# Performance work log

Measured on AMD Instinct MI355X. Metric: run time of the kernel, lower is better.

The kernel has to match this reference:

```python
import jax, jax.numpy as jnp
import numpy as np

N, E, HD, ED = 8000, 40000, 64, 16


def setup_inputs() -> dict:
    key = jax.random.key(0)
    ks = jax.random.split(key, 10)
    def nrm(k, shp, s):
        return jax.random.normal(k, shp, dtype=jnp.float32) * s
    return {
        "x": jax.random.normal(ks[0], (N, HD), dtype=jnp.float32),
        "edge_attr": jax.random.uniform(ks[1], (E, ED), dtype=jnp.float32),
        "W1": nrm(ks[2], (ED, HD), 0.2),
        "b1": jnp.zeros((HD,), jnp.float32),
        "W2": nrm(ks[3], (HD, HD * HD), 0.05),
        "b2": jnp.zeros((HD * HD,), jnp.float32),
        "W_root": nrm(ks[4], (HD, HD), 0.1),
        "b_conv": jnp.zeros((HD,), jnp.float32),
        "w_ih": nrm(ks[5], (3 * HD, HD), 0.1),
        "w_hh": nrm(ks[6], (3 * HD, HD), 0.1),
        "b_ih": jnp.zeros((3 * HD,), jnp.float32),
        "b_hh": jnp.zeros((3 * HD,), jnp.float32),
        "edge_index": jax.random.randint(ks[7], (2, E), 0, N),
    }


def reference(x, edge_attr, W1, b1, W2, b2, W_root, b_conv, w_ih, w_hh, b_ih, b_hh, edge_index):
    src, dst = edge_index[0], edge_index[1]
    n_nodes, hd = x.shape
    n_edges = edge_attr.shape[0]
    # in-degree counts for scatter-mean (guard against isolated nodes)
    counts = jnp.maximum(
        jax.ops.segment_sum(jnp.ones((n_edges,), x.dtype), dst, num_segments=n_nodes), 1.0
    )
    # edge MLP -> per-edge [hd, hd] weight; edge_attr is loop-invariant so compute once
    Wedge = (jax.nn.relu(edge_attr @ W1 + b1) @ W2 + b2).reshape(n_edges, hd, hd)

    def gru_cell(m, h):
        gi = m @ w_ih.T + b_ih  # [N, 3h], gate order r,z,n (torch layout)
        gh = h @ w_hh.T + b_hh
        i_r, i_z, i_n = jnp.split(gi, 3, axis=-1)
        h_r, h_z, h_n = jnp.split(gh, 3, axis=-1)
        r = jax.nn.sigmoid(i_r + h_r)
        z = jax.nn.sigmoid(i_z + h_z)
        n = jnp.tanh(i_n + r * h_n)
        return (1.0 - z) * n + z * h

    out = x
    hidden = x  # h = out.unsqueeze(0)
    for _ in range(3):
        # NNConv: gather source feats, per-edge matmul, scatter-mean to target
        msg = jnp.einsum('ei,eio->eo', out[src], Wedge)  # [E, hd]
        agg = jax.ops.segment_sum(msg, dst, num_segments=n_nodes) / counts[:, None]
        m = jax.nn.relu(agg + out @ W_root.T + b_conv)
        hidden = gru_cell(m, hidden)
        out = hidden  # GRU output == new hidden for seq_len 1
    return out
```

## Files before the change

kernel.cpp:

```cpp
#include <hip/hip_runtime.h>

#define HD 64
#define ED 16
#define NB 16
#define OSTR 144
#define NSTR 9232
#define LDSB (NB*NSTR)
#define GSTR 201

typedef __bf16 bf16x8 __attribute__((ext_vector_type(8)));
typedef float  f32x4  __attribute__((ext_vector_type(4)));
typedef unsigned int u32;
typedef unsigned long long u64;
typedef unsigned short u16;

static inline __device__ float bf2f(u16 u){
    union { u32 i; float f; } v; v.i = ((u32)u) << 16; return v.f;
}
static inline __device__ u16 f2bf(float f){
    union { u32 i; float f; } v; v.f = f;
    u32 r = v.i + 0x7FFF + ((v.i >> 16) & 1);
    return (u16)(r >> 16);
}
static inline __device__ u32 pk2(float a, float b){
    return (u32)f2bf(a) | ((u32)f2bf(b) << 16);
}

__global__ void k_zero2(int* a, int* b, int n){
    int i = blockIdx.x*blockDim.x + threadIdx.x;
    if(i < n){ a[i] = 0; b[i] = 0; }
}
__global__ void k_zerof(float* a, int n){
    int i = blockIdx.x*blockDim.x + threadIdx.x;
    if(i < n) a[i] = 0.f;
}
__global__ void k_deg(const int* __restrict__ src, const int* __restrict__ dst, int E,
                      int* __restrict__ degs, int* __restrict__ degd){
    int e = blockIdx.x*blockDim.x + threadIdx.x;
    if(e < E){ atomicAdd(&degs[src[e]], 1); atomicAdd(&degd[dst[e]], 1); }
}

__global__ void k_scan(const int* __restrict__ degs, const int* __restrict__ degd, int N,
                       int* __restrict__ rowptr, int* __restrict__ cursor, float* __restrict__ countsf){
    __shared__ int part[1024];
    int tid = threadIdx.x;
    int PER = (N + 1023) >> 10;
    int base = tid * PER;
    int local[16];
    int s = 0;
    for(int j = 0; j < PER; j++){
        int idx = base + j;
        int v = (idx < N) ? degs[idx] : 0;
        local[j] = s; s += v;
    }
    part[tid] = s;
    __syncthreads();
    for(int off = 1; off < 1024; off <<= 1){
        int v = (tid >= off) ? part[tid - off] : 0;
        __syncthreads();
        part[tid] += v;
        __syncthreads();
    }
    int prev = (tid == 0) ? 0 : part[tid - 1];
    for(int j = 0; j < PER; j++){
        int idx = base + j;
        if(idx < N){
            int r = prev + local[j];
            rowptr[idx] = r; cursor[idx] = r;
            int dd = degd[idx];
            countsf[idx] = (dd > 0) ? (float)dd : 1.0f;
        }
    }
    if(tid == 1023) rowptr[N] = prev + s;
}

__global__ void k_fill(const int* __restrict__ src, int E, int* __restrict__ cursor, int* __restrict__ elist){
    int e = blockIdx.x*blockDim.x + threadIdx.x;
    if(e < E){ int p = atomicAdd(&cursor[src[e]], 1); elist[p] = e; }
}

__global__ void k_h1E(const float* __restrict__ ea, const float* __restrict__ W1,
                      const float* __restrict__ b1, const int* __restrict__ elist,
                      const int* __restrict__ dstarr, int E,
                      u16* __restrict__ h1E, int* __restrict__ dstE){
    __shared__ float s_ea[4][ED];
    __shared__ int s_e[4];
    int t = threadIdx.x;
    int o = t & 63, el = t >> 6;
    int p = blockIdx.x*4 + el;
    if(t < 4){
        int pp = blockIdx.x*4 + t;
        s_e[t] = (pp < E) ? elist[pp] : 0;
    }
    __syncthreads();
    if(t < 4*ED){
        int pe = t/ED;
        s_ea[pe][t%ED] = ea[(size_t)s_e[pe]*ED + t%ED];
    }
    __syncthreads();
    if(p < E){
        float acc = b1[o];
        #pragma unroll
        for(int k = 0; k < ED; k++) acc += s_ea[el][k] * W1[k*HD + o];
        h1E[(size_t)p*HD + o] = f2bf(acc > 0.f ? acc : 0.f);
        if(o == 0) dstE[p] = dstarr[s_e[el]];
    }
}

__global__ void k_permT(const float* __restrict__ W2, const float* __restrict__ b2,
                        u16* __restrict__ PT){
    int idx = blockIdx.x*blockDim.x + threadIdx.x;
    if(idx >= 65*HD*HD) return;
    int c = idx / HD, i = idx % HD;
    int kc = c >> 6, o = c & 63;
    float v = (kc < HD) ? W2[(size_t)kc*(HD*HD) + i*HD + o] : b2[i*HD + o];
    PT[idx] = f2bf(v);
}

__global__ void k_cvtA(const float* __restrict__ s, u16* __restrict__ a, int n){
    int i = (blockIdx.x*blockDim.x + threadIdx.x) * 4;
    if(i < n){
        float4 v = *(const float4*)&s[i];
        ushort4 o;
        o.x = f2bf(v.x); o.y = f2bf(v.y); o.z = f2bf(v.z); o.w = f2bf(v.w);
        *(ushort4*)&a[i] = o;
    }
}

__global__ __launch_bounds__(1024) void k_fused(
        const u16* __restrict__ Abf, const u16* __restrict__ PT,
        const u16* __restrict__ h1E, const int* __restrict__ rowptr,
        const int* __restrict__ dstE, int E, float* __restrict__ agg){
    extern __shared__ char smem[];
    int t = threadIdx.x;
    int w = t >> 6;
    int lane = t & 63;
    int r = lane & 15, g = lane >> 4;
    int nb0 = blockIdx.x * NB;

    bf16x8 afr0 = *(const bf16x8*)&Abf[(size_t)(nb0 + r)*HD + g*8];
    bf16x8 afr1 = *(const bf16x8*)&Abf[(size_t)(nb0 + r)*HD + 32 + g*8];
    {
        f32x4 acc[4][4];
        #pragma unroll
        for(int j = 0; j < 4; j++)
            #pragma unroll
            for(int cb = 0; cb < 4; cb++) acc[j][cb] = (f32x4){0.f,0.f,0.f,0.f};
        #pragma unroll
        for(int j = 0; j < 4; j++){
            int kc = 4*w + j;
            const u16* Pb = PT + (size_t)kc*HD*HD;
            #pragma unroll
            for(int cb = 0; cb < 4; cb++){
                bf16x8 b0 = *(const bf16x8*)&Pb[(size_t)(cb*16 + r)*HD + g*8];
                bf16x8 b1 = *(const bf16x8*)&Pb[(size_t)(cb*16 + r)*HD + 32 + g*8];
                acc[j][cb] = __builtin_amdgcn_mfma_f32_16x16x32_bf16(afr0, b0, acc[j][cb], 0,0,0);
                acc[j][cb] = __builtin_amdgcn_mfma_f32_16x16x32_bf16(afr1, b1, acc[j][cb], 0,0,0);
            }
        }
        #pragma unroll
        for(int cb = 0; cb < 4; cb++){
            int o = cb*16 + r;
            int slotp = ((w>>1) + 2*o + (o>>3)) & 7;
            #pragma unroll
            for(int reg = 0; reg < 4; reg++){
                int node = 4*g + reg;
                u32 lo = pk2(acc[0][cb][reg], acc[1][cb][reg]);
                u32 hi = pk2(acc[2][cb][reg], acc[3][cb][reg]);
                *(u64*)(smem + node*NSTR + o*OSTR + slotp*16 + 8*(w&1)) =
                    (u64)lo | ((u64)hi << 32);
            }
        }
        if(w == 0){
            f32x4 accB[4];
            #pragma unroll
            for(int cb = 0; cb < 4; cb++) accB[cb] = (f32x4){0.f,0.f,0.f,0.f};
            const u16* Pb = PT + (size_t)64*HD*HD;
            #pragma unroll
            for(int cb = 0; cb < 4; cb++){
                bf16x8 b0 = *(const bf16x8*)&Pb[(size_t)(cb*16 + r)*HD + g*8];
                bf16x8 b1 = *(const bf16x8*)&Pb[(size_t)(cb*16 + r)*HD + 32 + g*8];
                accB[cb] = __builtin_amdgcn_mfma_f32_16x16x32_bf16(afr0, b0, accB[cb], 0,0,0);
                accB[cb] = __builtin_amdgcn_mfma_f32_16x16x32_bf16(afr1, b1, accB[cb], 0,0,0);
            }
            #pragma unroll
            for(int cb = 0; cb < 4; cb++)
                #pragma unroll
                for(int reg = 0; reg < 4; reg++)
                    *(u16*)(smem + (4*g+reg)*NSTR + (cb*16+r)*OSTR + 128) =
                        f2bf(accB[cb][reg]);
        }
    }
    __syncthreads();

    int s = nb0 + w;
    int beg = rowptr[s], end = rowptr[s+1];
    if(beg == end) return;
    const char* nodebase = smem + w*NSTR;
    bf16x8 sB[4][2];
    float bval[4];
    #pragma unroll
    for(int cb = 0; cb < 4; cb++){
        int o = cb*16 + r;
        #pragma unroll
        for(int ks = 0; ks < 2; ks++){
            int slotp = ((ks*4 + g) + 2*o + (o>>3)) & 7;
            sB[cb][ks] = *(const bf16x8*)(nodebase + o*OSTR + slotp*16);
        }
        bval[cb] = bf2f(*(const u16*)(nodebase + o*OSTR + 128));
    }
    for(int p0 = beg; p0 < end; p0 += 16){
        int p = p0 + r;
        int pc = p < E ? p : E-1;
        bf16x8 a0 = *(const bf16x8*)&h1E[(size_t)pc*HD + g*8];
        bf16x8 a1 = *(const bf16x8*)&h1E[(size_t)pc*HD + 32 + g*8];
        f32x4 acc2[4];
        #pragma unroll
        for(int cb = 0; cb < 4; cb++){
            acc2[cb] = (f32x4){0.f,0.f,0.f,0.f};
            acc2[cb] = __builtin_amdgcn_mfma_f32_16x16x32_bf16(a0, sB[cb][0], acc2[cb], 0,0,0);
            acc2[cb] = __builtin_amdgcn_mfma_f32_16x16x32_bf16(a1, sB[cb][1], acc2[cb], 0,0,0);
        }
        int dq[4];
        #pragma unroll
        for(int reg = 0; reg < 4; reg++){
            int q = p0 + 4*g + reg;
            dq[reg] = (q < end) ? dstE[q] : -1;
        }
        #pragma unroll
        for(int cb = 0; cb < 4; cb++)
            #pragma unroll
            for(int reg = 0; reg < 4; reg++)
                if(dq[reg] >= 0)
                    atomicAdd(&agg[(size_t)dq[reg]*HD + cb*16 + r],
                              acc2[cb][reg] + bval[cb]);
    }
}

__global__ __launch_bounds__(256) void k_mgru2(
        const float* __restrict__ agg, const float* __restrict__ countsf,
        const float* __restrict__ state, const u16* __restrict__ Abf,
        const u16* __restrict__ WrB,  const u16* __restrict__ WihB,
        const u16* __restrict__ WhhB, const float* __restrict__ bconv,
        const float* __restrict__ b_ih, const float* __restrict__ b_hh,
        float* __restrict__ hnew, u16* __restrict__ AbfN){
    __shared__ u16   s_mbf[16*72];
    __shared__ float s_gi[16*GSTR];
    __shared__ float s_gh[16*GSTR];
    int t = threadIdx.x;
    int w = t >> 6, lane = t & 63;
    int r = lane & 15, g = lane >> 4;
    int n0 = blockIdx.x * 16;

    bf16x8 afr0 = *(const bf16x8*)&Abf[(size_t)(n0 + r)*HD + g*8];
    bf16x8 afr1 = *(const bf16x8*)&Abf[(size_t)(n0 + r)*HD + 32 + g*8];

    {
        float bc = bconv[w*16 + r];
        f32x4 accR = (f32x4){bc, bc, bc, bc};
        bf16x8 b0 = *(const bf16x8*)&WrB[(size_t)(w*16 + r)*HD + g*8];
        bf16x8 b1 = *(const bf16x8*)&WrB[(size_t)(w*16 + r)*HD + 32 + g*8];
        accR = __builtin_amdgcn_mfma_f32_16x16x32_bf16(afr0, b0, accR, 0,0,0);
        accR = __builtin_amdgcn_mfma_f32_16x16x32_bf16(afr1, b1, accR, 0,0,0);
        #pragma unroll
        for(int reg = 0; reg < 4; reg++){
            int row = 4*g + reg;
            float cnt = countsf[n0 + row];
            float m = agg[(size_t)(n0 + row)*HD + w*16 + r] / cnt + accR[reg];
            s_mbf[row*72 + w*16 + r] = f2bf(m > 0.f ? m : 0.f);
        }
    }
    __syncthreads();

    bf16x8 am0 = *(const bf16x8*)&s_mbf[r*72 + g*8];
    bf16x8 am1 = *(const bf16x8*)&s_mbf[r*72 + 32 + g*8];

    #pragma unroll
    for(int j = 0; j < 3; j++){
        int cb = w + 4*j;
        int col = cb*16 + r;
        float bi = b_ih[col];
        f32x4 acc = (f32x4){bi, bi, bi, bi};
        bf16x8 b0 = *(const bf16x8*)&WihB[(size_t)col*HD + g*8];
        bf16x8 b1 = *(const bf16x8*)&WihB[(size_t)col*HD + 32 + g*8];
        acc = __builtin_amdgcn_mfma_f32_16x16x32_bf16(am0, b0, acc, 0,0,0);
        acc = __builtin_amdgcn_mfma_f32_16x16x32_bf16(am1, b1, acc, 0,0,0);
        #pragma unroll
        for(int reg = 0; reg < 4; reg++)
            s_gi[(4*g + reg)*GSTR + col] = acc[reg];
    }
    #pragma unroll
    for(int j = 0; j < 3; j++){
        int cb = w + 4*j;
        int col = cb*16 + r;
        float bh = b_hh[col];
        f32x4 acc = (f32x4){bh, bh, bh, bh};
        bf16x8 b0 = *(const bf16x8*)&WhhB[(size_t)col*HD + g*8];
        bf16x8 b1 = *(const bf16x8*)&WhhB[(size_t)col*HD + 32 + g*8];
        acc = __builtin_amdgcn_mfma_f32_16x16x32_bf16(afr0, b0, acc, 0,0,0);
        acc = __builtin_amdgcn_mfma_f32_16x16x32_bf16(afr1, b1, acc, 0,0,0);
        #pragma unroll
        for(int reg = 0; reg < 4; reg++)
            s_gh[(4*g + reg)*GSTR + col] = acc[reg];
    }
    __syncthreads();

    #pragma unroll
    for(int q = 0; q < 4; q++){
        int idx = t + q*256;
        int nl = idx >> 6, o = idx & 63;
        const float* gi = s_gi + nl*GSTR;
        const float* gh = s_gh + nl*GSTR;
        float rr  = 1.f/(1.f + __expf(-(gi[o]      + gh[o])));
        float zz  = 1.f/(1.f + __expf(-(gi[64+o]   + gh[64+o])));
        float nnv = tanhf(gi[128+o] + rr*gh[128+o]);
        float xo = state[(size_t)(n0+nl)*HD + o];
        float h = (1.f - zz)*nnv + zz*xo;
        hnew[(size_t)(n0+nl)*HD + o] = h;
        AbfN[(size_t)(n0+nl)*HD + o] = f2bf(h);
    }
}

extern "C" void kernel_launch(void* const* d_in, const int* in_sizes, int n_in,
                              void* d_out, int out_size, void* d_ws, size_t ws_size,
                              hipStream_t stream){
    const float* x     = (const float*)d_in[0];
    const float* ea    = (const float*)d_in[1];
    const float* W1    = (const float*)d_in[2];
    const float* b1    = (const float*)d_in[3];
    const float* W2    = (const float*)d_in[4];
    const float* b2    = (const float*)d_in[5];
    const float* Wroot = (const float*)d_in[6];
    const float* bconv = (const float*)d_in[7];
    const float* w_ih  = (const float*)d_in[8];
    const float* w_hh  = (const float*)d_in[9];
    const float* b_ih  = (const float*)d_in[10];
    const float* b_hh  = (const float*)d_in[11];
    const int*   eidx  = (const int*)d_in[12];
    int N = in_sizes[0] / HD;
    int E = in_sizes[1] / ED;
    const int* srcarr = eidx;
    const int* dstarr = eidx + E;

    char* w = (char*)d_ws;
    size_t off = 0;
    auto alloc = [&](size_t bytes)->char*{
        char* p = w + off; off = (off + bytes + 255) & ~(size_t)255; return p;
    };
    int*   deg_src = (int*)alloc((size_t)N*4);
    int*   deg_dst = (int*)alloc((size_t)N*4);
    int*   rowptr  = (int*)alloc((size_t)(N+1)*4);
    int*   cursor  = (int*)alloc((size_t)N*4);
    int*   elist   = (int*)alloc((size_t)E*4);
    int*   dstE    = (int*)alloc((size_t)E*4);
    float* countsf = (float*)alloc((size_t)N*4);
    u16*   h1E     = (u16*)alloc((size_t)E*HD*2);
    u16*   PT      = (u16*)alloc((size_t)65*HD*HD*2);
    u16*   Abf     = (u16*)alloc((size_t)N*HD*2);
    u16*   WihB    = (u16*)alloc((size_t)3*HD*HD*2);
    u16*   WhhB    = (u16*)alloc((size_t)3*HD*HD*2);
    u16*   WrB     = (u16*)alloc((size_t)HD*HD*2);
    float* agg     = (float*)alloc((size_t)N*HD*4);
    float* stA     = (float*)alloc((size_t)N*HD*4);
    float* stB     = (float*)alloc((size_t)N*HD*4);

    hipFuncSetAttribute((const void*)k_fused,
                        hipFuncAttributeMaxDynamicSharedMemorySize, LDSB);

    hipLaunchKernelGGL(k_zero2, dim3((N+255)/256), dim3(256), 0, stream, deg_src, deg_dst, N);
    hipLaunchKernelGGL(k_deg,   dim3((E+255)/256), dim3(256), 0, stream, srcarr, dstarr, E, deg_src, deg_dst);
    hipLaunchKernelGGL(k_scan,  dim3(1), dim3(1024), 0, stream, deg_src, deg_dst, N, rowptr, cursor, countsf);
    hipLaunchKernelGGL(k_fill,  dim3((E+255)/256), dim3(256), 0, stream, srcarr, E, cursor, elist);
    hipLaunchKernelGGL(k_h1E,   dim3((E+3)/4), dim3(256), 0, stream, ea, W1, b1, elist, dstarr, E, h1E, dstE);
    hipLaunchKernelGGL(k_permT, dim3((65*HD*HD+255)/256), dim3(256), 0, stream, W2, b2, PT);
    hipLaunchKernelGGL(k_cvtA,  dim3((3*HD*HD/4+255)/256), dim3(256), 0, stream, w_ih, WihB, 3*HD*HD);
    hipLaunchKernelGGL(k_cvtA,  dim3((3*HD*HD/4+255)/256), dim3(256), 0, stream, w_hh, WhhB, 3*HD*HD);
    hipLaunchKernelGGL(k_cvtA,  dim3((HD*HD/4+255)/256), dim3(256), 0, stream, Wroot, WrB, HD*HD);
    hipLaunchKernelGGL(k_cvtA,  dim3((N*HD/4+255)/256), dim3(256), 0, stream, x, Abf, N*HD);

    const float* state = x;
    for(int it = 0; it < 3; ++it){
        hipLaunchKernelGGL(k_zerof, dim3((N*HD+255)/256), dim3(256), 0, stream, agg, N*HD);
        hipLaunchKernelGGL(k_fused, dim3(N/NB), dim3(1024), LDSB, stream,
                           Abf, PT, h1E, rowptr, dstE, E, agg);
        float* outp = (it == 2) ? (float*)d_out : ((it == 0) ? stA : stB);
        hipLaunchKernelGGL(k_mgru2, dim3(N/16), dim3(256), 0, stream,
                           agg, countsf, state, Abf, WrB, WihB, WhhB,
                           bconv, b_ih, b_hh, outp, Abf);
        state = outp;
    }
}
```

Measured before the change: 222.1 us.

## Split fused NNConv kernel across two K-halves with 512-thread blocks

```diff
diff --git a/kernel.cpp b/kernel.cpp
--- a/kernel.cpp
+++ b/kernel.cpp
@@ -3,10 +3,9 @@
 #define HD 64
 #define ED 16
 #define NB 16
-#define OSTR 144
-#define NSTR 9232
-#define LDSB (NB*NSTR)
-#define GSTR 201
+#define OSTR2 72
+#define NSTR2 4616
+#define LDS2B (NB*NSTR2 + NB*HD*4)
 
 typedef __bf16 bf16x8 __attribute__((ext_vector_type(8)));
 typedef float  f32x4  __attribute__((ext_vector_type(4)));
@@ -127,16 +126,24 @@
     }
 }
 
-__global__ __launch_bounds__(1024) void k_fused(
+__global__ __launch_bounds__(512, 4) void k_fused2(
         const u16* __restrict__ Abf, const u16* __restrict__ PT,
         const u16* __restrict__ h1E, const int* __restrict__ rowptr,
         const int* __restrict__ dstE, int E, float* __restrict__ agg){
     extern __shared__ char smem[];
+    float* s_biasf = (float*)(smem + NB*NSTR2);
     int t = threadIdx.x;
     int w = t >> 6;
     int lane = t & 63;
     int r = lane & 15, g = lane >> 4;
-    int nb0 = blockIdx.x * NB;
+    int gb = blockIdx.x;
+    int grp = gb >> 1, h = gb & 1;
+    int nb0 = grp * NB;
+
+    int n0 = 2*w, n1 = 2*w + 1;
+    int beg0 = rowptr[nb0 + n0];
+    int beg1 = rowptr[nb0 + n1];
+    int end1 = rowptr[nb0 + n1 + 1];
 
     bf16x8 afr0 = *(const bf16x8*)&Abf[(size_t)(nb0 + r)*HD + g*8];
     bf16x8 afr1 = *(const bf16x8*)&Abf[(size_t)(nb0 + r)*HD + 32 + g*8];
@@ -148,7 +155,7 @@
             for(int cb = 0; cb < 4; cb++) acc[j][cb] = (f32x4){0.f,0.f,0.f,0.f};
         #pragma unroll
         for(int j = 0; j < 4; j++){
-            int kc = 4*w + j;
+            int kc = h*32 + 4*w + j;
             const u16* Pb = PT + (size_t)kc*HD*HD;
             #pragma unroll
             for(int cb = 0; cb < 4; cb++){
@@ -161,17 +168,16 @@
         #pragma unroll
         for(int cb = 0; cb < 4; cb++){
             int o = cb*16 + r;
-            int slotp = ((w>>1) + 2*o + (o>>3)) & 7;
             #pragma unroll
             for(int reg = 0; reg < 4; reg++){
                 int node = 4*g + reg;
                 u32 lo = pk2(acc[0][cb][reg], acc[1][cb][reg]);
                 u32 hi = pk2(acc[2][cb][reg], acc[3][cb][reg]);
-                *(u64*)(smem + node*NSTR + o*OSTR + slotp*16 + 8*(w&1)) =
+                *(u64*)(smem + node*NSTR2 + o*OSTR2 + w*8) =
                     (u64)lo | ((u64)hi << 32);
             }
         }
-        if(w == 0){
+        if(h == 1 && w == 0){
             f32x4 accB[4];
             #pragma unroll
             for(int cb = 0; cb < 4; cb++) accB[cb] = (f32x4){0.f,0.f,0.f,0.f};
@@ -187,56 +193,53 @@
             for(int cb = 0; cb < 4; cb++)
                 #pragma unroll
                 for(int reg = 0; reg < 4; reg++)
-                    *(u16*)(smem + (4*g+reg)*NSTR + (cb*16+r)*OSTR + 128) =
-                        f2bf(accB[cb][reg]);
-        }
-    }
-    __syncthreads();
-
-    int s = nb0 + w;
-    int beg = rowptr[s], end = rowptr[s+1];
-    if(beg == end) return;
-    const char* nodebase = smem + w*NSTR;
-    bf16x8 sB[4][2];
-    float bval[4];
+                    s_biasf[(4*g + reg)*HD + cb*16 + r] = accB[cb][reg];
+        }
+    }
+    __syncthreads();
+
     #pragma unroll
-    for(int cb = 0; cb < 4; cb++){
-        int o = cb*16 + r;
-        #pragma unroll
-        for(int ks = 0; ks < 2; ks++){
-            int slotp = ((ks*4 + g) + 2*o + (o>>3)) & 7;
-            sB[cb][ks] = *(const bf16x8*)(nodebase + o*OSTR + slotp*16);
-        }
-        bval[cb] = bf2f(*(const u16*)(nodebase + o*OSTR + 128));
-    }
-    for(int p0 = beg; p0 < end; p0 += 16){
-        int p = p0 + r;
-        int pc = p < E ? p : E-1;
-        bf16x8 a0 = *(const bf16x8*)&h1E[(size_t)pc*HD + g*8];
-        bf16x8 a1 = *(const bf16x8*)&h1E[(size_t)pc*HD + 32 + g*8];
-        f32x4 acc2[4];
+    for(int nn = 0; nn < 2; nn++){
+        int node = (nn == 0) ? n0 : n1;
+        int beg  = (nn == 0) ? beg0 : beg1;
+        int end  = (nn == 0) ? beg1 : end1;
+        if(beg == end) continue;
+        const char* nodebase = smem + node*NSTR2;
+        bf16x8 sB[4];
+        float bval[4];
         #pragma unroll
         for(int cb = 0; cb < 4; cb++){
-            acc2[cb] = (f32x4){0.f,0.f,0.f,0.f};
-            acc2[cb] = __builtin_amdgcn_mfma_f32_16x16x32_bf16(a0, sB[cb][0], acc2[cb], 0,0,0);
-            acc2[cb] = __builtin_amdgcn_mfma_f32_16x16x32_bf16(a1, sB[cb][1], acc2[cb], 0,0,0);
-        }
-        int dq[4];
-        #pragma unroll
-        for(int reg = 0; reg < 4; reg++){
-            int q = p0 + 4*g + reg;
-            dq[reg] = (q < end) ? dstE[q] : -1;
-        }
-        #pragma unroll
-        for(int cb = 0; cb < 4; cb++)
-            #pragma unroll
-            for(int reg = 0; reg < 4; reg++)
-                if(dq[reg] >= 0)
-                    atomicAdd(&agg[(size_t)dq[reg]*HD + cb*16 + r],
-                              acc2[cb][reg] + bval[cb]);
-    }
-}
-
+            sB[cb] = *(const bf16x8*)(nodebase + (cb*16 + r)*OSTR2 + g*16);
+            bval[cb] = (h == 1) ? s_biasf[node*HD + cb*16 + r] : 0.f;
+        }
+        for(int p0 = beg; p0 < end; p0 += 16){
+            int p = p0 + r;
+            int pc = p < E ? p : E-1;
+            bf16x8 a0 = *(const bf16x8*)&h1E[(size_t)pc*HD + h*32 + g*8];
+            f32x4 acc2[4];
+            #pragma unroll
+            for(int cb = 0; cb < 4; cb++){
+                acc2[cb] = (f32x4){0.f,0.f,0.f,0.f};
+                acc2[cb] = __builtin_amdgcn_mfma_f32_16x16x32_bf16(a0, sB[cb], acc2[cb], 0,0,0);
+            }
+            int dq[4];
+            #pragma unroll
+            for(int reg = 0; reg < 4; reg++){
+                int q = p0 + 4*g + reg;
+                dq[reg] = (q < end) ? dstE[q] : -1;
+            }
+            #pragma unroll
+            for(int cb = 0; cb < 4; cb++)
+                #pragma unroll
+                for(int reg = 0; reg < 4; reg++)
+                    if(dq[reg] >= 0)
+                        atomicAdd(&agg[(size_t)dq[reg]*HD + cb*16 + r],
+                                  acc2[cb][reg] + bval[cb]);
+        }
+    }
+}
+
+#define GSTR 201
 __global__ __launch_bounds__(256) void k_mgru2(
         const float* __restrict__ agg, const float* __restrict__ countsf,
         const float* __restrict__ state, const u16* __restrict__ Abf,
@@ -315,9 +318,9 @@
         float zz  = 1.f/(1.f + __expf(-(gi[64+o]   + gh[64+o])));
         float nnv = tanhf(gi[128+o] + rr*gh[128+o]);
         float xo = state[(size_t)(n0+nl)*HD + o];
-        float h = (1.f - zz)*nnv + zz*xo;
-        hnew[(size_t)(n0+nl)*HD + o] = h;
-        AbfN[(size_t)(n0+nl)*HD + o] = f2bf(h);
+        float hh = (1.f - zz)*nnv + zz*xo;
+        hnew[(size_t)(n0+nl)*HD + o] = hh;
+        AbfN[(size_t)(n0+nl)*HD + o] = f2bf(hh);
     }
 }
 
@@ -364,8 +367,8 @@
     float* stA     = (float*)alloc((size_t)N*HD*4);
     float* stB     = (float*)alloc((size_t)N*HD*4);
 
-    hipFuncSetAttribute((const void*)k_fused,
-                        hipFuncAttributeMaxDynamicSharedMemorySize, LDSB);
+    hipFuncSetAttribute((const void*)k_fused2,
+                        hipFuncAttributeMaxDynamicSharedMemorySize, LDS2B);
 
     hipLaunchKernelGGL(k_zero2, dim3((N+255)/256), dim3(256), 0, stream, deg_src, deg_dst, N);
     hipLaunchKernelGGL(k_deg,   dim3((E+255)/256), dim3(256), 0, stream, srcarr, dstarr, E, deg_src, deg_dst);
@@ -381,7 +384,7 @@
     const float* state = x;
     for(int it = 0; it < 3; ++it){
         hipLaunchKernelGGL(k_zerof, dim3((N*HD+255)/256), dim3(256), 0, stream, agg, N*HD);
-        hipLaunchKernelGGL(k_fused, dim3(N/NB), dim3(1024), LDSB, stream,
+        hipLaunchKernelGGL(k_fused2, dim3((N/NB)*2), dim3(512), LDS2B, stream,
                            Abf, PT, h1E, rowptr, dstE, E, agg);
         float* outp = (it == 2) ? (float*)d_out : ((it == 0) ? stA : stB);
         hipLaunchKernelGGL(k_mgru2, dim3(N/16), dim3(256), 0, stream,
```

Result: no change. 226.1 us (+1.8%).

## Split fused per-node GEMM and message kernel, staging node matrices in global memory

Applied to the files above, without the earlier changes.

```diff
diff --git a/kernel.cpp b/kernel.cpp
--- a/kernel.cpp
+++ b/kernel.cpp
@@ -2,11 +2,6 @@
 
 #define HD 64
 #define ED 16
-#define NB 16
-#define OSTR 144
-#define NSTR 9232
-#define LDSB (NB*NSTR)
-#define GSTR 201
 
 typedef __bf16 bf16x8 __attribute__((ext_vector_type(8)));
 typedef float  f32x4  __attribute__((ext_vector_type(4)));
@@ -127,87 +122,93 @@
     }
 }
 
-__global__ __launch_bounds__(1024) void k_fused(
+__global__ __launch_bounds__(256) void k_gemmA(
         const u16* __restrict__ Abf, const u16* __restrict__ PT,
+        u16* __restrict__ Mt){
+    int t = threadIdx.x;
+    int w = t >> 6, lane = t & 63;
+    int r = lane & 15, g = lane >> 4;
+    int kcq = blockIdx.x;
+    int n0 = (blockIdx.y * 4 + w) * 16;
+
+    bf16x8 a0 = *(const bf16x8*)&Abf[(size_t)(n0 + r)*HD + g*8];
+    bf16x8 a1 = *(const bf16x8*)&Abf[(size_t)(n0 + r)*HD + 32 + g*8];
+
+    f32x4 acc[8][4];
+    #pragma unroll
+    for(int j = 0; j < 8; j++)
+        #pragma unroll
+        for(int cb = 0; cb < 4; cb++) acc[j][cb] = (f32x4){0.f,0.f,0.f,0.f};
+
+    #pragma unroll
+    for(int j = 0; j < 8; j++){
+        const u16* Pb = PT + (size_t)(kcq*8 + j)*HD*HD;
+        #pragma unroll
+        for(int cb = 0; cb < 4; cb++){
+            bf16x8 b0 = *(const bf16x8*)&Pb[(cb*16 + r)*HD + g*8];
+            bf16x8 b1 = *(const bf16x8*)&Pb[(cb*16 + r)*HD + 32 + g*8];
+            acc[j][cb] = __builtin_amdgcn_mfma_f32_16x16x32_bf16(a0, b0, acc[j][cb], 0,0,0);
+            acc[j][cb] = __builtin_amdgcn_mfma_f32_16x16x32_bf16(a1, b1, acc[j][cb], 0,0,0);
+        }
+    }
+
+    #pragma unroll
+    for(int cb = 0; cb < 4; cb++)
+        #pragma unroll
+        for(int reg = 0; reg < 4; reg++){
+            int node = n0 + 4*g + reg;
+            uint4 val;
+            val.x = pk2(acc[0][cb][reg], acc[1][cb][reg]);
+            val.y = pk2(acc[2][cb][reg], acc[3][cb][reg]);
+            val.z = pk2(acc[4][cb][reg], acc[5][cb][reg]);
+            val.w = pk2(acc[6][cb][reg], acc[7][cb][reg]);
+            *(uint4*)&Mt[(size_t)node*4096 + (size_t)(kcq*64 + cb*16 + r)*8] = val;
+        }
+}
+
+__global__ __launch_bounds__(256) void k_biasA(
+        const u16* __restrict__ Abf, const u16* __restrict__ PT,
+        float* __restrict__ Mb){
+    int t = threadIdx.x;
+    int w = t >> 6, lane = t & 63;
+    int r = lane & 15, g = lane >> 4;
+    int n0 = (blockIdx.x * 4 + w) * 16;
+    bf16x8 a0 = *(const bf16x8*)&Abf[(size_t)(n0 + r)*HD + g*8];
+    bf16x8 a1 = *(const bf16x8*)&Abf[(size_t)(n0 + r)*HD + 32 + g*8];
+    const u16* Pb = PT + (size_t)64*HD*HD;
+    #pragma unroll
+    for(int cb = 0; cb < 4; cb++){
+        f32x4 acc = (f32x4){0.f,0.f,0.f,0.f};
+        bf16x8 b0 = *(const bf16x8*)&Pb[(cb*16 + r)*HD + g*8];
+        bf16x8 b1 = *(const bf16x8*)&Pb[(cb*16 + r)*HD + 32 + g*8];
+        acc = __builtin_amdgcn_mfma_f32_16x16x32_bf16(a0, b0, acc, 0,0,0);
+        acc = __builtin_amdgcn_mfma_f32_16x16x32_bf16(a1, b1, acc, 0,0,0);
+        #pragma unroll
+        for(int reg = 0; reg < 4; reg++)
+            Mb[(size_t)(n0 + 4*g + reg)*HD + cb*16 + r] = acc[reg];
+    }
+}
+
+__global__ __launch_bounds__(256) void k_msgB(
+        const u16* __restrict__ Mt, const float* __restrict__ Mb,
         const u16* __restrict__ h1E, const int* __restrict__ rowptr,
         const int* __restrict__ dstE, int E, float* __restrict__ agg){
-    extern __shared__ char smem[];
-    int t = threadIdx.x;
-    int w = t >> 6;
-    int lane = t & 63;
+    int t = threadIdx.x;
+    int w = t >> 6, lane = t & 63;
     int r = lane & 15, g = lane >> 4;
-    int nb0 = blockIdx.x * NB;
-
-    bf16x8 afr0 = *(const bf16x8*)&Abf[(size_t)(nb0 + r)*HD + g*8];
-    bf16x8 afr1 = *(const bf16x8*)&Abf[(size_t)(nb0 + r)*HD + 32 + g*8];
-    {
-        f32x4 acc[4][4];
-        #pragma unroll
-        for(int j = 0; j < 4; j++)
-            #pragma unroll
-            for(int cb = 0; cb < 4; cb++) acc[j][cb] = (f32x4){0.f,0.f,0.f,0.f};
-        #pragma unroll
-        for(int j = 0; j < 4; j++){
-            int kc = 4*w + j;
-            const u16* Pb = PT + (size_t)kc*HD*HD;
-            #pragma unroll
-            for(int cb = 0; cb < 4; cb++){
-                bf16x8 b0 = *(const bf16x8*)&Pb[(size_t)(cb*16 + r)*HD + g*8];
-                bf16x8 b1 = *(const bf16x8*)&Pb[(size_t)(cb*16 + r)*HD + 32 + g*8];
-                acc[j][cb] = __builtin_amdgcn_mfma_f32_16x16x32_bf16(afr0, b0, acc[j][cb], 0,0,0);
-                acc[j][cb] = __builtin_amdgcn_mfma_f32_16x16x32_bf16(afr1, b1, acc[j][cb], 0,0,0);
-            }
-        }
-        #pragma unroll
-        for(int cb = 0; cb < 4; cb++){
-            int o = cb*16 + r;
-            int slotp = ((w>>1) + 2*o + (o>>3)) & 7;
-            #pragma unroll
-            for(int reg = 0; reg < 4; reg++){
-                int node = 4*g + reg;
-                u32 lo = pk2(acc[0][cb][reg], acc[1][cb][reg]);
-                u32 hi = pk2(acc[2][cb][reg], acc[3][cb][reg]);
-                *(u64*)(smem + node*NSTR + o*OSTR + slotp*16 + 8*(w&1)) =
-                    (u64)lo | ((u64)hi << 32);
-            }
-        }
-        if(w == 0){
-            f32x4 accB[4];
-            #pragma unroll
-            for(int cb = 0; cb < 4; cb++) accB[cb] = (f32x4){0.f,0.f,0.f,0.f};
-            const u16* Pb = PT + (size_t)64*HD*HD;
-            #pragma unroll
-            for(int cb = 0; cb < 4; cb++){
-                bf16x8 b0 = *(const bf16x8*)&Pb[(size_t)(cb*16 + r)*HD + g*8];
-                bf16x8 b1 = *(const bf16x8*)&Pb[(size_t)(cb*16 + r)*HD + 32 + g*8];
-                accB[cb] = __builtin_amdgcn_mfma_f32_16x16x32_bf16(afr0, b0, accB[cb], 0,0,0);
-                accB[cb] = __builtin_amdgcn_mfma_f32_16x16x32_bf16(afr1, b1, accB[cb], 0,0,0);
-            }
-            #pragma unroll
-            for(int cb = 0; cb < 4; cb++)
-                #pragma unroll
-                for(int reg = 0; reg < 4; reg++)
-                    *(u16*)(smem + (4*g+reg)*NSTR + (cb*16+r)*OSTR + 128) =
-                        f2bf(accB[cb][reg]);
-        }
-    }
-    __syncthreads();
-
-    int s = nb0 + w;
+    int s = blockIdx.x * 4 + w;
     int beg = rowptr[s], end = rowptr[s+1];
     if(beg == end) return;
-    const char* nodebase = smem + w*NSTR;
+
+    const u16* Mn = Mt + (size_t)s*4096;
     bf16x8 sB[4][2];
     float bval[4];
     #pragma unroll
     for(int cb = 0; cb < 4; cb++){
-        int o = cb*16 + r;
-        #pragma unroll
-        for(int ks = 0; ks < 2; ks++){
-            int slotp = ((ks*4 + g) + 2*o + (o>>3)) & 7;
-            sB[cb][ks] = *(const bf16x8*)(nodebase + o*OSTR + slotp*16);
-        }
-        bval[cb] = bf2f(*(const u16*)(nodebase + o*OSTR + 128));
+        #pragma unroll
+        for(int ks = 0; ks < 2; ks++)
+            sB[cb][ks] = *(const bf16x8*)&Mn[(size_t)((ks*4 + g)*64 + cb*16 + r)*8];
+        bval[cb] = Mb[(size_t)s*HD + cb*16 + r];
     }
     for(int p0 = beg; p0 < end; p0 += 16){
         int p = p0 + r;
@@ -237,6 +238,7 @@
     }
 }
 
+#define GSTR 201
 __global__ __launch_bounds__(256) void k_mgru2(
         const float* __restrict__ agg, const float* __restrict__ countsf,
         const float* __restrict__ state, const u16* __restrict__ Abf,
@@ -315,9 +317,9 @@
         float zz  = 1.f/(1.f + __expf(-(gi[64+o]   + gh[64+o])));
         float nnv = tanhf(gi[128+o] + rr*gh[128+o]);
         float xo = state[(size_t)(n0+nl)*HD + o];
-        float h = (1.f - zz)*nnv + zz*xo;
-        hnew[(size_t)(n0+nl)*HD + o] = h;
-        AbfN[(size_t)(n0+nl)*HD + o] = f2bf(h);
+        float hh = (1.f - zz)*nnv + zz*xo;
+        hnew[(size_t)(n0+nl)*HD + o] = hh;
+        AbfN[(size_t)(n0+nl)*HD + o] = f2bf(hh);
     }
 }
 
@@ -363,9 +365,8 @@
     float* agg     = (float*)alloc((size_t)N*HD*4);
     float* stA     = (float*)alloc((size_t)N*HD*4);
     float* stB     = (float*)alloc((size_t)N*HD*4);
-
-    hipFuncSetAttribute((const void*)k_fused,
-                        hipFuncAttributeMaxDynamicSharedMemorySize, LDSB);
+    float* Mb      = (float*)alloc((size_t)N*HD*4);
+    u16*   Mt      = (u16*)alloc((size_t)N*4096*2);
 
     hipLaunchKernelGGL(k_zero2, dim3((N+255)/256), dim3(256), 0, stream, deg_src, deg_dst, N);
     hipLaunchKernelGGL(k_deg,   dim3((E+255)/256), dim3(256), 0, stream, srcarr, dstarr, E, deg_src, deg_dst);
@@ -381,8 +382,10 @@
     const float* state = x;
     for(int it = 0; it < 3; ++it){
         hipLaunchKernelGGL(k_zerof, dim3((N*HD+255)/256), dim3(256), 0, stream, agg, N*HD);
-        hipLaunchKernelGGL(k_fused, dim3(N/NB), dim3(1024), LDSB, stream,
-                           Abf, PT, h1E, rowptr, dstE, E, agg);
+        hipLaunchKernelGGL(k_gemmA, dim3(8, N/64), dim3(256), 0, stream, Abf, PT, Mt);
+        hipLaunchKernelGGL(k_biasA, dim3(N/64), dim3(256), 0, stream, Abf, PT, Mb);
+        hipLaunchKernelGGL(k_msgB,  dim3(N/4), dim3(256), 0, stream,
+                           Mt, Mb, h1E, rowptr, dstE, E, agg);
         float* outp = (it == 2) ? (float*)d_out : ((it == 0) ? stA : stB);
         hipLaunchKernelGGL(k_mgru2, dim3(N/16), dim3(256), 0, stream,
                            agg, countsf, state, Abf, WrB, WihB, WhhB,
```

After: 273.6 us. +23.2%, slower.
